# Kernel tuning notes

Hardware: AMD Instinct MI355X
Metric: run time of the kernel (lower is better)

Reference implementation:

```python
import jax, jax.numpy as jnp
import numpy as np

B = 32768    # number of trees (batch)
N = 10       # nodes per tree (forced by Linear(embed_dim*10, ...))
L = 10       # leaf tokens per subtree (also 10, same cat constraint)
E = 16       # embed_dim
H = 8        # hidden_dim
V = 2000     # embed_dict_size
LAT = 128    # latent_vector_dim
EPS = 1e-5   # BatchNorm1d eps


def setup_inputs() -> dict:
    key = jax.random.key(0)
    ks = jax.random.split(key, 17)
    w = lambda k, shape, s=0.05: (jax.random.normal(k, shape, jnp.float32) * s)
    return {
        "tokens": jax.random.randint(ks[0], (B, N, L), 0, V),
        "emb":    w(ks[1], (V, E), 0.1),            # nn.Embedding weight
        "w_ih":   w(ks[2], (4 * E, E)),             # LSTM input weights (i,f,g,o)
        "b_ih":   w(ks[3], (4 * E,)),
        "b_hh":   w(ks[4], (4 * E,)),               # h0=c0=0 so W_hh never contributes
        "ffW1":   w(ks[5], (4 * E, 10 * E)),        # child_sum_ff Linear(160,64)
        "ffb1":   w(ks[6], (4 * E,)),
        "ffW2":   w(ks[7], (E, 4 * E)),             # child_sum_ff Linear(64,16)
        "ffb2":   w(ks[8], (E,)),
        "fmW":    w(ks[9], (H, E)),                 # ff_model Linear(16,8)
        "fmb":    w(ks[10], (H,)),
        "tsW":    w(ks[11], (1, H)),                # tail_score Linear(8,1)
        "tsb":    w(ks[12], (1,)),
        "suW":    w(ks[13], (LAT, H)),              # tail_summary Linear(8,latent)
        "sub_b":  w(ks[14], (LAT,)),
        "gamma":  jnp.ones((LAT,), jnp.float32),    # BatchNorm1d affine
        "beta":   jnp.zeros((LAT,), jnp.float32),
    }


def _child_ff(x, W1, b1, W2, b2):
    # nn.Sequential(Linear(160,64), ReLU, Linear(64,16))
    return jax.nn.relu(x @ W1.T + b1) @ W2.T + b2


def _lstm_single_step(x, w_ih, b_ih, b_hh):
    # One-timestep LSTM with zero initial (h, c); PyTorch gate order i,f,g,o.
    gates = x @ w_ih.T + b_ih + b_hh
    i, f, g, o = jnp.split(gates, 4, axis=-1)
    c = jax.nn.sigmoid(i) * jnp.tanh(g)          # f * c0 = 0
    return jax.nn.sigmoid(o) * jnp.tanh(c)


def reference(tokens, emb, w_ih, b_ih, b_hh, ffW1, ffb1, ffW2, ffb2,
              fmW, fmb, tsW, tsb, suW, sub_b, gamma, beta):
    leaf = emb[tokens]                                        # (B,N,L,E) gather
    subtree = _child_ff(leaf.reshape(B, N, L * E),
                        ffW1, ffb1, ffW2, ffb2)               # (B,N,E)
    h = _lstm_single_step(subtree, w_ih, b_ih, b_hh)          # (B,N,E)
    code = _child_ff(h.reshape(B, N * E), ffW1, ffb1, ffW2, ffb2)  # (B,E)
    ff_out = code @ fmW.T + fmb                               # (B,H)
    score = jnp.tanh(ff_out @ tsW.T + tsb)                    # (B,1)
    s = ff_out @ suW.T + sub_b                                # (B,LAT)
    mu = jnp.mean(s, axis=0)
    var = jnp.var(s, axis=0)                                  # biased, training-mode BN
    summary = gamma * (s - mu) / jnp.sqrt(var + EPS) + beta
    return score, summary
```

## Files before the change

### kernel.cpp

```cpp
#include <hip/hip_runtime.h>
#include <hip/hip_bf16.h>

#define BB 32768
#define NN 10
#define VV 2000
#define EPSBN 1e-5

__global__ __launch_bounds__(256) void k_table(const float* __restrict__ emb,
                                               const float* __restrict__ W1,
                                               float* __restrict__ T1) {
  int idx = blockIdx.x * 256 + threadIdx.x;
  if (idx >= VV * 640) return;
  int v = idx / 640;
  int r = idx - v * 640;
  int l = r >> 6;
  int o = r & 63;
  const float* e = emb + v * 16;
  const float* w = W1 + o * 160 + l * 16;
  float s = 0.f;
#pragma unroll
  for (int k = 0; k < 16; ++k) s = fmaf(e[k], w[k], s);
  T1[idx] = s;
}

__global__ __launch_bounds__(256) void k_fuse(const float* __restrict__ w_ih,
    const float* __restrict__ b_ih, const float* __restrict__ b_hh,
    const float* __restrict__ W2, const float* __restrict__ b2v,
    float* __restrict__ W3, float* __restrict__ bias3) {
  int idx = blockIdx.x * 256 + threadIdx.x;
  if (idx < 4096) {
    int j = idx >> 6, k = idx & 63;
    float s = 0.f;
#pragma unroll
    for (int o = 0; o < 16; ++o) s = fmaf(w_ih[j * 16 + o], W2[o * 64 + k], s);
    W3[idx] = s;
  } else if (idx < 4160) {
    int j = idx - 4096;
    float s = b_ih[j] + b_hh[j];
#pragma unroll
    for (int o = 0; o < 16; ++o) s = fmaf(w_ih[j * 16 + o], b2v[o], s);
    bias3[j] = s;
  }
}

__global__ __launch_bounds__(256) void k_stage1(const int* __restrict__ tokens,
    const float* __restrict__ T1, const float* __restrict__ b1v,
    const float* __restrict__ W3, const float* __restrict__ bias3,
    float* __restrict__ hbuf) {
  __shared__ float lds[4][64];
  const int tid = threadIdx.x;
  const int lane = tid & 63;
  const int wid = tid >> 6;
  float* wl = lds[wid];
  float w3r[64];
#pragma unroll
  for (int k = 0; k < 64; k += 4) {
    float4 v = *(const float4*)&W3[lane * 64 + k];
    w3r[k] = v.x; w3r[k + 1] = v.y; w3r[k + 2] = v.z; w3r[k + 3] = v.w;
  }
  const float b1l = b1v[lane];
  const float b3l = bias3[lane];
  const bool isG = ((lane >> 4) == 2);
  const int gw = blockIdx.x * 4 + wid;

  int item = gw;
  int tokv = (lane < 10) ? tokens[item * 10 + lane] : 0;
  float t[10];
#pragma unroll
  for (int l = 0; l < 10; ++l) {
    int tv = __builtin_amdgcn_readlane(tokv, l);
    t[l] = T1[tv * 640 + l * 64 + lane];
  }
  tokv = (lane < 10) ? tokens[(item + 8192) * 10 + lane] : 0;

  for (int iter = 0; iter < 40; ++iter) {
    float h1 = b1l;
#pragma unroll
    for (int l = 0; l < 10; ++l) h1 += t[l];
    h1 = fmaxf(h1, 0.f);
    wl[lane] = h1;
    __builtin_amdgcn_wave_barrier();

    {
      int tok_n = tokv;
      int nxt2 = item + 16384;
      int src = (nxt2 < BB * NN) ? nxt2 : item;
      tokv = (lane < 10) ? tokens[src * 10 + lane] : 0;
#pragma unroll
      for (int l = 0; l < 10; ++l) {
        int tv = __builtin_amdgcn_readlane(tok_n, l);
        t[l] = T1[tv * 640 + l * 64 + lane];
      }
    }

    float g = b3l;
#pragma unroll
    for (int k = 0; k < 64; k += 4) {
      float4 hv = *(const float4*)&wl[k];
      g = fmaf(w3r[k],     hv.x, g);
      g = fmaf(w3r[k + 1], hv.y, g);
      g = fmaf(w3r[k + 2], hv.z, g);
      g = fmaf(w3r[k + 3], hv.w, g);
    }

    float e = __expf(isG ? -2.f * g : -g);
    float r = 1.f / (1.f + e);
    float act = isG ? fmaf(2.f, r, -1.f) : r;

    int sl = lane & 15;
    float ga = __shfl(act, sl + 32);
    float oa = __shfl(act, sl + 48);
    if (lane < 16) {
      float c = act * ga;
      float e2 = __expf(-2.f * c);
      float th = fmaf(2.f, 1.f / (1.f + e2), -1.f);
      hbuf[item * 16 + lane] = oa * th;
    }
    __builtin_amdgcn_wave_barrier();
    item += 8192;
  }
}

__global__ __launch_bounds__(256) void k_stage2(const float* __restrict__ hbuf,
    const float* __restrict__ W1, const float* __restrict__ b1v,
    const float* __restrict__ W2, const float* __restrict__ b2v,
    const float* __restrict__ fmW, const float* __restrict__ fmb,
    const float* __restrict__ tsW, const float* __restrict__ tsb,
    const float* __restrict__ suW, const float* __restrict__ sub_b,
    float* __restrict__ out, float* __restrict__ partials) {
  __shared__ float h1b_lds[32 * 68];
  __shared__ float code_lds[32 * 20];
  __shared__ float ff_lds[32 * 12];
  int tid = threadIdx.x;
  int lane = tid & 63;
  int wid = __builtin_amdgcn_readfirstlane(tid >> 6);
  int treeBase = blockIdx.x * 32;
  {
    int tw = treeBase + wid * 8;
    float acc[8];
#pragma unroll
    for (int t = 0; t < 8; ++t) acc[t] = b1v[lane];
    const float* wrow = W1 + lane * 160;
    const float* xbase = hbuf + (size_t)tw * 160;
    for (int k = 0; k < 160; k += 4) {
      float4 wv = *(const float4*)(wrow + k);
#pragma unroll
      for (int t = 0; t < 8; ++t) {
        float4 xv = *(const float4*)(xbase + t * 160 + k);
        acc[t] = fmaf(wv.x, xv.x, acc[t]);
        acc[t] = fmaf(wv.y, xv.y, acc[t]);
        acc[t] = fmaf(wv.z, xv.z, acc[t]);
        acc[t] = fmaf(wv.w, xv.w, acc[t]);
      }
    }
#pragma unroll
    for (int t = 0; t < 8; ++t)
      h1b_lds[(wid * 8 + t) * 68 + lane] = fmaxf(acc[t], 0.f);
  }
  __syncthreads();
  {
    int t2 = tid >> 3, jj = tid & 7;
    float c0 = b2v[jj], c1 = b2v[jj + 8];
    const float* w2a = W2 + jj * 64;
    const float* w2b = W2 + (jj + 8) * 64;
    const float* hb = &h1b_lds[t2 * 68];
    for (int o = 0; o < 64; o += 4) {
      float4 hv = *(const float4*)(hb + o);
      float4 a4 = *(const float4*)(w2a + o);
      float4 b4 = *(const float4*)(w2b + o);
      c0 = fmaf(a4.x, hv.x, c0); c0 = fmaf(a4.y, hv.y, c0);
      c0 = fmaf(a4.z, hv.z, c0); c0 = fmaf(a4.w, hv.w, c0);
      c1 = fmaf(b4.x, hv.x, c1); c1 = fmaf(b4.y, hv.y, c1);
      c1 = fmaf(b4.z, hv.z, c1); c1 = fmaf(b4.w, hv.w, c1);
    }
    code_lds[t2 * 20 + jj] = c0;
    code_lds[t2 * 20 + jj + 8] = c1;
  }
  __syncthreads();
  {
    int t = tid >> 3, q = tid & 7;
    float f = fmb[q];
    const float* cw = fmW + q * 16;
    const float* cl = &code_lds[t * 20];
#pragma unroll
    for (int j4 = 0; j4 < 16; j4 += 4) {
      float4 cv = *(const float4*)(cl + j4);
      float4 wv = *(const float4*)(cw + j4);
      f = fmaf(wv.x, cv.x, f); f = fmaf(wv.y, cv.y, f);
      f = fmaf(wv.z, cv.z, f); f = fmaf(wv.w, cv.w, f);
    }
    ff_lds[t * 12 + q] = f;
  }
  __syncthreads();
  {
    int t = tid >> 3, r = tid & 7;
    float4 f0 = *(const float4*)&ff_lds[t * 12];
    float4 f1 = *(const float4*)&ff_lds[t * 12 + 4];
    int tree = treeBase + t;
    float* od = out + (size_t)BB + (size_t)tree * 128 + r * 16;
#pragma unroll
    for (int cc = 0; cc < 16; ++cc) {
      int c = r * 16 + cc;
      const float* u = suW + c * 8;
      float4 u0 = *(const float4*)(u);
      float4 u1 = *(const float4*)(u + 4);
      float sv = sub_b[c];
      sv = fmaf(u0.x, f0.x, sv); sv = fmaf(u0.y, f0.y, sv);
      sv = fmaf(u0.z, f0.z, sv); sv = fmaf(u0.w, f0.w, sv);
      sv = fmaf(u1.x, f1.x, sv); sv = fmaf(u1.y, f1.y, sv);
      sv = fmaf(u1.z, f1.z, sv); sv = fmaf(u1.w, f1.w, sv);
      od[cc] = sv;
    }
    if (tid < 32) {
      int tt = tid;
      float4 g0 = *(const float4*)&ff_lds[tt * 12];
      float4 g1 = *(const float4*)&ff_lds[tt * 12 + 4];
      float sc = tsb[0];
      sc = fmaf(tsW[0], g0.x, sc); sc = fmaf(tsW[1], g0.y, sc);
      sc = fmaf(tsW[2], g0.z, sc); sc = fmaf(tsW[3], g0.w, sc);
      sc = fmaf(tsW[4], g1.x, sc); sc = fmaf(tsW[5], g1.y, sc);
      sc = fmaf(tsW[6], g1.z, sc); sc = fmaf(tsW[7], g1.w, sc);
      out[treeBase + tt] = tanhf(sc);
    }
  }
  {
    int waveId = blockIdx.x * 4 + wid;
    float* pw = partials + (size_t)waveId * 88;
#pragma unroll
    for (int rep = 0; rep < 2; ++rep) {
      int e = lane + rep * 64;
      if (e < 81) {
        int i = e / 9, jx = e - i * 9;
        float m = 0.f;
#pragma unroll
        for (int t = 0; t < 8; ++t) {
          const float* fr = &ff_lds[(wid * 8 + t) * 12];
          float fi = (i  < 8) ? fr[i]  : 1.f;
          float fj = (jx < 8) ? fr[jx] : 1.f;
          m = fmaf(fi, fj, m);
        }
        pw[e] = m;
      }
    }
  }
}

__global__ __launch_bounds__(256) void k_reduce(const float* __restrict__ partials,
                                                double* __restrict__ Msum) {
  __shared__ double red[256];
  int e = blockIdx.x;
  double s = 0.0;
  for (int w = threadIdx.x; w < 4096; w += 256)
    s += (double)partials[(size_t)w * 88 + e];
  red[threadIdx.x] = s;
  __syncthreads();
  for (int off = 128; off > 0; off >>= 1) {
    if (threadIdx.x < off) red[threadIdx.x] += red[threadIdx.x + off];
    __syncthreads();
  }
  if (threadIdx.x == 0) Msum[e] = red[0];
}

__global__ __launch_bounds__(128) void k_stats(const double* __restrict__ Msum,
    const float* __restrict__ suW, const float* __restrict__ sub_b,
    const float* __restrict__ gamma, const float* __restrict__ beta,
    float* __restrict__ statsA, float* __restrict__ statsB) {
  int c = threadIdx.x;
  double u[9];
#pragma unroll
  for (int q = 0; q < 8; ++q) u[q] = (double)suW[c * 8 + q];
  u[8] = (double)sub_b[c];
  double S1 = 0.0;
#pragma unroll
  for (int i = 0; i < 9; ++i) S1 += u[i] * Msum[72 + i];
  double mu = S1 / (double)BB;
  double E2 = 0.0;
#pragma unroll
  for (int i = 0; i < 9; ++i) {
    double acc = 0.0;
#pragma unroll
    for (int jx = 0; jx < 9; ++jx) acc += u[jx] * Msum[i * 9 + jx];
    E2 += u[i] * acc;
  }
  E2 /= (double)BB;
  double var = E2 - mu * mu;
  if (var < 0.0) var = 0.0;
  double rs = 1.0 / sqrt(var + (double)EPSBN);
  double A = (double)gamma[c] * rs;
  statsA[c] = (float)A;
  statsB[c] = (float)((double)beta[c] - mu * A);
}

__global__ __launch_bounds__(256) void k_norm(float* __restrict__ out,
    const float* __restrict__ statsA, const float* __restrict__ statsB) {
  int idx = blockIdx.x * 256 + threadIdx.x;
  float4* p = (float4*)(out + BB);
  float4 v = p[idx];
  int c4 = idx & 31;
  float4 a = ((const float4*)statsA)[c4];
  float4 b = ((const float4*)statsB)[c4];
  v.x = fmaf(v.x, a.x, b.x);
  v.y = fmaf(v.y, a.y, b.y);
  v.z = fmaf(v.z, a.z, b.z);
  v.w = fmaf(v.w, a.w, b.w);
  p[idx] = v;
}

extern "C" void kernel_launch(void* const* d_in, const int* in_sizes, int n_in,
                              void* d_out, int out_size, void* d_ws, size_t ws_size,
                              hipStream_t stream) {
  const int*   tokens = (const int*)d_in[0];
  const float* emb   = (const float*)d_in[1];
  const float* w_ih  = (const float*)d_in[2];
  const float* b_ih  = (const float*)d_in[3];
  const float* b_hh  = (const float*)d_in[4];
  const float* ffW1  = (const float*)d_in[5];
  const float* ffb1  = (const float*)d_in[6];
  const float* ffW2  = (const float*)d_in[7];
  const float* ffb2  = (const float*)d_in[8];
  const float* fmW   = (const float*)d_in[9];
  const float* fmb   = (const float*)d_in[10];
  const float* tsW   = (const float*)d_in[11];
  const float* tsb   = (const float*)d_in[12];
  const float* suW   = (const float*)d_in[13];
  const float* sub_b = (const float*)d_in[14];
  const float* gamma = (const float*)d_in[15];
  const float* beta  = (const float*)d_in[16];
  float* out = (float*)d_out;
  float* ws = (float*)d_ws;

  float*  T1       = ws;
  float*  hbuf     = T1 + 1280000;
  float*  partials = hbuf + 5242880;
  double* Msum     = (double*)(partials + 360448);
  float*  statsA   = (float*)(Msum + 82);
  float*  statsB   = statsA + 128;
  float*  W3       = statsB + 128;
  float*  bias3    = W3 + 4096;

  hipLaunchKernelGGL(k_table,  dim3(5000), dim3(256), 0, stream, emb, ffW1, T1);
  hipLaunchKernelGGL(k_fuse,   dim3(17),   dim3(256), 0, stream,
                     w_ih, b_ih, b_hh, ffW2, ffb2, W3, bias3);
  hipLaunchKernelGGL(k_stage1, dim3(2048), dim3(256), 0, stream,
                     tokens, T1, ffb1, W3, bias3, hbuf);
  hipLaunchKernelGGL(k_stage2, dim3(1024), dim3(256), 0, stream,
                     hbuf, ffW1, ffb1, ffW2, ffb2, fmW, fmb, tsW, tsb, suW, sub_b,
                     out, partials);
  hipLaunchKernelGGL(k_reduce, dim3(81),   dim3(256), 0, stream, partials, Msum);
  hipLaunchKernelGGL(k_stats,  dim3(1),    dim3(128), 0, stream,
                     Msum, suW, sub_b, gamma, beta, statsA, statsB);
  hipLaunchKernelGGL(k_norm,   dim3(4096), dim3(256), 0, stream, out, statsA, statsB);
}
```

Baseline: 195.5 us.

## Double-buffer stage1 gathers with two items in flight and more waves

Restructures the stage-1 node kernel so each wave holds two independent items (tA/tB) and prefetches tokens two items ahead. Token indices are now loaded as uniform scalar loads instead of readlane broadcasts. The grid doubles to 16384 waves with 20 items each, and the launch bounds ask for 4 blocks per CU. Reciprocals switch to the hardware rcp, and an asm barrier pins the W3 weights in registers. The goal is to hide the T1 gather latency; the cost is higher register pressure, which could reduce occupancy or cause spills.

```diff
diff --git a/kernel.cpp b/kernel.cpp
--- a/kernel.cpp
+++ b/kernel.cpp
@@ -43,81 +43,99 @@
   }
 }
 
-__global__ __launch_bounds__(256) void k_stage1(const int* __restrict__ tokens,
+#define K1_WAVES 16384
+#define K1_ITEMS 20
+
+#define K1_STEP(ITEM, T, TOK, NIDX)                                        \
+  {                                                                        \
+    float h1 = b1l;                                                        \
+    _Pragma("unroll") for (int l = 0; l < 10; ++l) h1 += T[l];             \
+    h1 = fmaxf(h1, 0.f);                                                   \
+    wl[lane] = h1;                                                         \
+    __builtin_amdgcn_wave_barrier();                                       \
+    _Pragma("unroll") for (int l = 0; l < 10; ++l) {                       \
+      T[l] = T1[TOK[l] * 640 + l * 64 + lane];                             \
+    }                                                                      \
+    {                                                                      \
+      int ci = (NIDX) < BB * NN ? (NIDX) : 0;                              \
+      const int* tpn = tokens + (size_t)ci * 10;                           \
+      _Pragma("unroll") for (int l = 0; l < 10; ++l) TOK[l] = tpn[l];      \
+    }                                                                      \
+    float g = b3l;                                                         \
+    _Pragma("unroll") for (int k = 0; k < 64; k += 4) {                    \
+      float4 hv = *(const float4*)&wl[k];                                  \
+      g = fmaf(w3r[k],     hv.x, g);                                       \
+      g = fmaf(w3r[k + 1], hv.y, g);                                       \
+      g = fmaf(w3r[k + 2], hv.z, g);                                       \
+      g = fmaf(w3r[k + 3], hv.w, g);                                       \
+    }                                                                      \
+    float e = __expf(isG ? -2.f * g : -g);                                 \
+    float r = __builtin_amdgcn_rcpf(1.f + e);                              \
+    float act = isG ? fmaf(2.f, r, -1.f) : r;                              \
+    int sl = lane & 15;                                                    \
+    float ga = __shfl(act, sl + 32);                                       \
+    float oa = __shfl(act, sl + 48);                                       \
+    if (lane < 16) {                                                       \
+      float c = act * ga;                                                  \
+      float e2 = __expf(-2.f * c);                                         \
+      float th = fmaf(2.f, __builtin_amdgcn_rcpf(1.f + e2), -1.f);         \
+      hbuf[(size_t)(ITEM) * 16 + lane] = oa * th;                          \
+    }                                                                      \
+    __builtin_amdgcn_wave_barrier();                                       \
+  }
+
+__global__ __launch_bounds__(256, 4) void k_stage1(const int* __restrict__ tokens,
     const float* __restrict__ T1, const float* __restrict__ b1v,
     const float* __restrict__ W3, const float* __restrict__ bias3,
     float* __restrict__ hbuf) {
   __shared__ float lds[4][64];
   const int tid = threadIdx.x;
   const int lane = tid & 63;
-  const int wid = tid >> 6;
+  const int wid = __builtin_amdgcn_readfirstlane(tid >> 6);
   float* wl = lds[wid];
+
   float w3r[64];
 #pragma unroll
   for (int k = 0; k < 64; k += 4) {
     float4 v = *(const float4*)&W3[lane * 64 + k];
     w3r[k] = v.x; w3r[k + 1] = v.y; w3r[k + 2] = v.z; w3r[k + 3] = v.w;
   }
+#pragma unroll
+  for (int k = 0; k < 64; ++k) asm volatile("" : "+v"(w3r[k]));
+
   const float b1l = b1v[lane];
   const float b3l = bias3[lane];
   const bool isG = ((lane >> 4) == 2);
-  const int gw = blockIdx.x * 4 + wid;
-
-  int item = gw;
-  int tokv = (lane < 10) ? tokens[item * 10 + lane] : 0;
-  float t[10];
-#pragma unroll
-  for (int l = 0; l < 10; ++l) {
-    int tv = __builtin_amdgcn_readlane(tokv, l);
-    t[l] = T1[tv * 640 + l * 64 + lane];
-  }
-  tokv = (lane < 10) ? tokens[(item + 8192) * 10 + lane] : 0;
-
-  for (int iter = 0; iter < 40; ++iter) {
-    float h1 = b1l;
-#pragma unroll
-    for (int l = 0; l < 10; ++l) h1 += t[l];
-    h1 = fmaxf(h1, 0.f);
-    wl[lane] = h1;
-    __builtin_amdgcn_wave_barrier();
-
-    {
-      int tok_n = tokv;
-      int nxt2 = item + 16384;
-      int src = (nxt2 < BB * NN) ? nxt2 : item;
-      tokv = (lane < 10) ? tokens[src * 10 + lane] : 0;
-#pragma unroll
-      for (int l = 0; l < 10; ++l) {
-        int tv = __builtin_amdgcn_readlane(tok_n, l);
-        t[l] = T1[tv * 640 + l * 64 + lane];
-      }
-    }
-
-    float g = b3l;
-#pragma unroll
-    for (int k = 0; k < 64; k += 4) {
-      float4 hv = *(const float4*)&wl[k];
-      g = fmaf(w3r[k],     hv.x, g);
-      g = fmaf(w3r[k + 1], hv.y, g);
-      g = fmaf(w3r[k + 2], hv.z, g);
-      g = fmaf(w3r[k + 3], hv.w, g);
-    }
-
-    float e = __expf(isG ? -2.f * g : -g);
-    float r = 1.f / (1.f + e);
-    float act = isG ? fmaf(2.f, r, -1.f) : r;
-
-    int sl = lane & 15;
-    float ga = __shfl(act, sl + 32);
-    float oa = __shfl(act, sl + 48);
-    if (lane < 16) {
-      float c = act * ga;
-      float e2 = __expf(-2.f * c);
-      float th = fmaf(2.f, 1.f / (1.f + e2), -1.f);
-      hbuf[item * 16 + lane] = oa * th;
-    }
-    __builtin_amdgcn_wave_barrier();
-    item += 8192;
+  const int gw = __builtin_amdgcn_readfirstlane(blockIdx.x * 4 + wid);
+
+  int tokA[10], tokB[10];
+  float tA[10], tB[10];
+  {
+    const int* t0 = tokens + (size_t)gw * 10;
+    const int* t1 = tokens + (size_t)(gw + K1_WAVES) * 10;
+#pragma unroll
+    for (int l = 0; l < 10; ++l) tokA[l] = t0[l];
+#pragma unroll
+    for (int l = 0; l < 10; ++l) tokB[l] = t1[l];
+  }
+#pragma unroll
+  for (int l = 0; l < 10; ++l) tA[l] = T1[tokA[l] * 640 + l * 64 + lane];
+#pragma unroll
+  for (int l = 0; l < 10; ++l) tB[l] = T1[tokB[l] * 640 + l * 64 + lane];
+  {
+    const int* t2 = tokens + (size_t)(gw + 2 * K1_WAVES) * 10;
+    const int* t3 = tokens + (size_t)(gw + 3 * K1_WAVES) * 10;
+#pragma unroll
+    for (int l = 0; l < 10; ++l) tokA[l] = t2[l];
+#pragma unroll
+    for (int l = 0; l < 10; ++l) tokB[l] = t3[l];
+  }
+
+#pragma unroll 1
+  for (int it = 0; it < K1_ITEMS; it += 2) {
+    int item = gw + it * K1_WAVES;
+    K1_STEP(item, tA, tokA, gw + (it + 4) * K1_WAVES);
+    K1_STEP(item + K1_WAVES, tB, tokB, gw + (it + 5) * K1_WAVES);
   }
 }
 
@@ -341,7 +359,7 @@
   hipLaunchKernelGGL(k_table,  dim3(5000), dim3(256), 0, stream, emb, ffW1, T1);
   hipLaunchKernelGGL(k_fuse,   dim3(17),   dim3(256), 0, stream,
                      w_ih, b_ih, b_hh, ffW2, ffb2, W3, bias3);
-  hipLaunchKernelGGL(k_stage1, dim3(2048), dim3(256), 0, stream,
+  hipLaunchKernelGGL(k_stage1, dim3(4096), dim3(256), 0, stream,
                      tokens, T1, ffb1, W3, bias3, hbuf);
   hipLaunchKernelGGL(k_stage2, dim3(1024), dim3(256), 0, stream,
                      hbuf, ffW1, ffb1, ffW2, ffb2, fmW, fmb, tsW, tsb, suW, sub_b,
```

New measurement: 186.5 us. 1.05x faster.

## Map one subtree item per thread in stage1 and drop the unused forget gate

Applied to the files above, without the earlier changes.

Stage1 moves from one wave per item, where lanes hold hidden units and share activations through LDS and shuffles, to one thread per item. Each thread gathers full 64-wide T1 rows with float4 loads, computes the 48 needed gate outputs (the forget gate is dropped from the fused weights) and writes 16 outputs with vector stores. This removes LDS traffic, wave barriers and cross-lane shuffles and cuts gate work by a quarter. In exchange each lane reads 640-float scattered rows, so gather coalescing gets worse. Register pressure is also high (64 h1 plus accumulators), and the W3T reads are uniform broadcast loads.

```diff
diff --git a/kernel.cpp b/kernel.cpp
--- a/kernel.cpp
+++ b/kernel.cpp
@@ -26,98 +26,106 @@
 __global__ __launch_bounds__(256) void k_fuse(const float* __restrict__ w_ih,
     const float* __restrict__ b_ih, const float* __restrict__ b_hh,
     const float* __restrict__ W2, const float* __restrict__ b2v,
-    float* __restrict__ W3, float* __restrict__ bias3) {
+    float* __restrict__ W3T, float* __restrict__ bias3T) {
   int idx = blockIdx.x * 256 + threadIdx.x;
-  if (idx < 4096) {
-    int j = idx >> 6, k = idx & 63;
+  if (idx < 3072) {
+    int k = idx / 48, jj = idx - k * 48;
+    int gr = (jj < 16) ? jj : jj + 16;
     float s = 0.f;
 #pragma unroll
-    for (int o = 0; o < 16; ++o) s = fmaf(w_ih[j * 16 + o], W2[o * 64 + k], s);
-    W3[idx] = s;
-  } else if (idx < 4160) {
-    int j = idx - 4096;
-    float s = b_ih[j] + b_hh[j];
-#pragma unroll
-    for (int o = 0; o < 16; ++o) s = fmaf(w_ih[j * 16 + o], b2v[o], s);
-    bias3[j] = s;
-  }
-}
-
-__global__ __launch_bounds__(256) void k_stage1(const int* __restrict__ tokens,
+    for (int o = 0; o < 16; ++o) s = fmaf(w_ih[gr * 16 + o], W2[o * 64 + k], s);
+    W3T[idx] = s;
+  } else if (idx < 3120) {
+    int jj = idx - 3072;
+    int gr = (jj < 16) ? jj : jj + 16;
+    float s = b_ih[gr] + b_hh[gr];
+#pragma unroll
+    for (int o = 0; o < 16; ++o) s = fmaf(w_ih[gr * 16 + o], b2v[o], s);
+    bias3T[jj] = s;
+  }
+}
+
+__global__ __launch_bounds__(64, 2) void k_stage1(const int* __restrict__ tokens,
     const float* __restrict__ T1, const float* __restrict__ b1v,
-    const float* __restrict__ W3, const float* __restrict__ bias3,
+    const float* __restrict__ W3T, const float* __restrict__ bias3T,
     float* __restrict__ hbuf) {
-  __shared__ float lds[4][64];
-  const int tid = threadIdx.x;
-  const int lane = tid & 63;
-  const int wid = tid >> 6;
-  float* wl = lds[wid];
-  float w3r[64];
-#pragma unroll
-  for (int k = 0; k < 64; k += 4) {
-    float4 v = *(const float4*)&W3[lane * 64 + k];
-    w3r[k] = v.x; w3r[k + 1] = v.y; w3r[k + 2] = v.z; w3r[k + 3] = v.w;
-  }
-  const float b1l = b1v[lane];
-  const float b3l = bias3[lane];
-  const bool isG = ((lane >> 4) == 2);
-  const int gw = blockIdx.x * 4 + wid;
-
-  int item = gw;
-  int tokv = (lane < 10) ? tokens[item * 10 + lane] : 0;
-  float t[10];
-#pragma unroll
-  for (int l = 0; l < 10; ++l) {
-    int tv = __builtin_amdgcn_readlane(tokv, l);
-    t[l] = T1[tv * 640 + l * 64 + lane];
-  }
-  tokv = (lane < 10) ? tokens[(item + 8192) * 10 + lane] : 0;
-
-  for (int iter = 0; iter < 40; ++iter) {
-    float h1 = b1l;
-#pragma unroll
-    for (int l = 0; l < 10; ++l) h1 += t[l];
-    h1 = fmaxf(h1, 0.f);
-    wl[lane] = h1;
-    __builtin_amdgcn_wave_barrier();
-
+  const int lane = threadIdx.x;
+#pragma unroll 1
+  for (int b = 0; b < 2; ++b) {
+    const int item = (blockIdx.x * 2 + b) * 64 + lane;
+    const int* tp = tokens + (size_t)item * 10;
+    int tok[10];
+#pragma unroll
+    for (int l = 0; l < 10; ++l) tok[l] = tp[l];
+
+    float4 h[16];
     {
-      int tok_n = tokv;
-      int nxt2 = item + 16384;
-      int src = (nxt2 < BB * NN) ? nxt2 : item;
-      tokv = (lane < 10) ? tokens[src * 10 + lane] : 0;
-#pragma unroll
-      for (int l = 0; l < 10; ++l) {
-        int tv = __builtin_amdgcn_readlane(tok_n, l);
-        t[l] = T1[tv * 640 + l * 64 + lane];
-      }
-    }
-
-    float g = b3l;
-#pragma unroll
-    for (int k = 0; k < 64; k += 4) {
-      float4 hv = *(const float4*)&wl[k];
-      g = fmaf(w3r[k],     hv.x, g);
-      g = fmaf(w3r[k + 1], hv.y, g);
-      g = fmaf(w3r[k + 2], hv.z, g);
-      g = fmaf(w3r[k + 3], hv.w, g);
-    }
-
-    float e = __expf(isG ? -2.f * g : -g);
-    float r = 1.f / (1.f + e);
-    float act = isG ? fmaf(2.f, r, -1.f) : r;
-
-    int sl = lane & 15;
-    float ga = __shfl(act, sl + 32);
-    float oa = __shfl(act, sl + 48);
-    if (lane < 16) {
-      float c = act * ga;
+      const float4* r = (const float4*)(T1 + (size_t)tok[0] * 640);
+#pragma unroll
+      for (int c = 0; c < 16; ++c) h[c] = r[c];
+    }
+#pragma unroll
+    for (int l = 1; l < 10; ++l) {
+      const float4* r = (const float4*)(T1 + (size_t)tok[l] * 640 + l * 64);
+#pragma unroll
+      for (int c = 0; c < 16; ++c) {
+        float4 v = r[c];
+        h[c].x += v.x; h[c].y += v.y; h[c].z += v.z; h[c].w += v.w;
+      }
+    }
+    float h1[64];
+    const float4* b1q = (const float4*)b1v;
+#pragma unroll
+    for (int c = 0; c < 16; ++c) {
+      float4 bq = b1q[c];
+      h1[4 * c]     = fmaxf(h[c].x + bq.x, 0.f);
+      h1[4 * c + 1] = fmaxf(h[c].y + bq.y, 0.f);
+      h1[4 * c + 2] = fmaxf(h[c].z + bq.z, 0.f);
+      h1[4 * c + 3] = fmaxf(h[c].w + bq.w, 0.f);
+    }
+
+    float acti[16], actg[16], acto[16];
+#pragma unroll
+    for (int ch = 0; ch < 3; ++ch) {
+      float acc[16];
+#pragma unroll
+      for (int j = 0; j < 16; ++j) acc[j] = bias3T[ch * 16 + j];
+#pragma unroll
+      for (int k = 0; k < 64; ++k) {
+        const float hk = h1[k];
+#pragma unroll
+        for (int j = 0; j < 16; ++j)
+          acc[j] = fmaf(W3T[k * 48 + ch * 16 + j], hk, acc[j]);
+      }
+#pragma unroll
+      for (int j = 0; j < 16; ++j) {
+        float x = acc[j];
+        float a;
+        if (ch == 1) {
+          float e = __expf(-2.f * x);
+          a = fmaf(2.f, __builtin_amdgcn_rcpf(1.f + e), -1.f);
+        } else {
+          float e = __expf(-x);
+          a = __builtin_amdgcn_rcpf(1.f + e);
+        }
+        if (ch == 0) acti[j] = a;
+        else if (ch == 1) actg[j] = a;
+        else acto[j] = a;
+      }
+    }
+
+    float res[16];
+#pragma unroll
+    for (int j = 0; j < 16; ++j) {
+      float c = acti[j] * actg[j];
       float e2 = __expf(-2.f * c);
-      float th = fmaf(2.f, 1.f / (1.f + e2), -1.f);
-      hbuf[item * 16 + lane] = oa * th;
-    }
-    __builtin_amdgcn_wave_barrier();
-    item += 8192;
+      float th = fmaf(2.f, __builtin_amdgcn_rcpf(1.f + e2), -1.f);
+      res[j] = acto[j] * th;
+    }
+    float4* op = (float4*)(hbuf + (size_t)item * 16);
+#pragma unroll
+    for (int q = 0; q < 4; ++q)
+      op[q] = make_float4(res[4 * q], res[4 * q + 1], res[4 * q + 2], res[4 * q + 3]);
   }
 }
 
@@ -335,14 +343,14 @@
   double* Msum     = (double*)(partials + 360448);
   float*  statsA   = (float*)(Msum + 82);
   float*  statsB   = statsA + 128;
-  float*  W3       = statsB + 128;
-  float*  bias3    = W3 + 4096;
+  float*  W3T      = statsB + 128;
+  float*  bias3T   = W3T + 3072;
 
   hipLaunchKernelGGL(k_table,  dim3(5000), dim3(256), 0, stream, emb, ffW1, T1);
-  hipLaunchKernelGGL(k_fuse,   dim3(17),   dim3(256), 0, stream,
-                     w_ih, b_ih, b_hh, ffW2, ffb2, W3, bias3);
-  hipLaunchKernelGGL(k_stage1, dim3(2048), dim3(256), 0, stream,
-                     tokens, T1, ffb1, W3, bias3, hbuf);
+  hipLaunchKernelGGL(k_fuse,   dim3(13),   dim3(256), 0, stream,
+                     w_ih, b_ih, b_hh, ffW2, ffb2, W3T, bias3T);
+  hipLaunchKernelGGL(k_stage1, dim3(2560), dim3(64), 0, stream,
+                     tokens, T1, ffb1, W3T, bias3T, hbuf);
   hipLaunchKernelGGL(k_stage2, dim3(1024), dim3(256), 0, stream,
                      hbuf, ffW1, ffb1, ffW2, ffb2, fmW, fmb, tsW, tsb, suW, sub_b,
                      out, partials);
```

Result: slower. 384.1 us (+96.4%).

## Split stage1 into gather kernel and batched gate kernel, merge prep kernels

Applied to the files above, without the earlier changes.

Replaces the persistent stage-1 kernel with two kernels: one gathers and sums table rows with float4 loads into an h1 buffer (folding the b1 bias into the table), and one computes the LSTM gates for 8 items per wave, reusing each weight load across them. The two small precompute kernels are merged into one launch, and division is replaced with hardware reciprocal. This trades the fused register pipeline for an extra intermediate buffer (about 84 MB written and read back) in exchange for more parallelism and better weight reuse.

```diff
diff --git a/kernel.cpp b/kernel.cpp
--- a/kernel.cpp
+++ b/kernel.cpp
@@ -6,118 +6,109 @@
 #define VV 2000
 #define EPSBN 1e-5
 
-__global__ __launch_bounds__(256) void k_table(const float* __restrict__ emb,
-                                               const float* __restrict__ W1,
-                                               float* __restrict__ T1) {
+__global__ __launch_bounds__(256) void k_prep(const float* __restrict__ emb,
+    const float* __restrict__ W1, const float* __restrict__ b1v,
+    const float* __restrict__ w_ih, const float* __restrict__ b_ih,
+    const float* __restrict__ b_hh, const float* __restrict__ W2,
+    const float* __restrict__ b2v,
+    float* __restrict__ T1, float* __restrict__ W3R, float* __restrict__ bias3) {
+  if (blockIdx.x < 5000) {
+    int idx = blockIdx.x * 256 + threadIdx.x;
+    int v = idx / 640;
+    int r = idx - v * 640;
+    int l = r >> 6;
+    int o = r & 63;
+    const float* e = emb + v * 16;
+    const float* w = W1 + o * 160 + l * 16;
+    float s = (l == 0) ? b1v[o] : 0.f;
+#pragma unroll
+    for (int k = 0; k < 16; ++k) s = fmaf(e[k], w[k], s);
+    T1[idx] = s;
+  } else {
+    int idx = (blockIdx.x - 5000) * 256 + threadIdx.x;
+    if (idx < 4096) {
+      int j = idx >> 6, k = idx & 63;
+      float s = 0.f;
+#pragma unroll
+      for (int o = 0; o < 16; ++o) s = fmaf(w_ih[j * 16 + o], W2[o * 64 + k], s);
+      W3R[idx] = s;
+    } else if (idx < 4160) {
+      int j = idx - 4096;
+      float s = b_ih[j] + b_hh[j];
+#pragma unroll
+      for (int o = 0; o < 16; ++o) s = fmaf(w_ih[j * 16 + o], b2v[o], s);
+      bias3[j] = s;
+    }
+  }
+}
+
+__global__ __launch_bounds__(256) void k_h1(const int* __restrict__ tokens,
+    const float* __restrict__ T1, float* __restrict__ h1buf) {
   int idx = blockIdx.x * 256 + threadIdx.x;
-  if (idx >= VV * 640) return;
-  int v = idx / 640;
-  int r = idx - v * 640;
-  int l = r >> 6;
-  int o = r & 63;
-  const float* e = emb + v * 16;
-  const float* w = W1 + o * 160 + l * 16;
-  float s = 0.f;
-#pragma unroll
-  for (int k = 0; k < 16; ++k) s = fmaf(e[k], w[k], s);
-  T1[idx] = s;
-}
-
-__global__ __launch_bounds__(256) void k_fuse(const float* __restrict__ w_ih,
-    const float* __restrict__ b_ih, const float* __restrict__ b_hh,
-    const float* __restrict__ W2, const float* __restrict__ b2v,
-    float* __restrict__ W3, float* __restrict__ bias3) {
-  int idx = blockIdx.x * 256 + threadIdx.x;
-  if (idx < 4096) {
-    int j = idx >> 6, k = idx & 63;
-    float s = 0.f;
-#pragma unroll
-    for (int o = 0; o < 16; ++o) s = fmaf(w_ih[j * 16 + o], W2[o * 64 + k], s);
-    W3[idx] = s;
-  } else if (idx < 4160) {
-    int j = idx - 4096;
-    float s = b_ih[j] + b_hh[j];
-#pragma unroll
-    for (int o = 0; o < 16; ++o) s = fmaf(w_ih[j * 16 + o], b2v[o], s);
-    bias3[j] = s;
-  }
-}
-
-__global__ __launch_bounds__(256) void k_stage1(const int* __restrict__ tokens,
-    const float* __restrict__ T1, const float* __restrict__ b1v,
-    const float* __restrict__ W3, const float* __restrict__ bias3,
+  int item = idx >> 4, c4 = (idx & 15) * 4;
+  const int* tp = tokens + (size_t)item * 10;
+  float4 a;
+  {
+    const float4* r = (const float4*)(T1 + (size_t)tp[0] * 640 + c4);
+    a = *r;
+  }
+#pragma unroll
+  for (int l = 1; l < 10; ++l) {
+    const float4* r = (const float4*)(T1 + (size_t)tp[l] * 640 + l * 64 + c4);
+    float4 v = *r;
+    a.x += v.x; a.y += v.y; a.z += v.z; a.w += v.w;
+  }
+  a.x = fmaxf(a.x, 0.f); a.y = fmaxf(a.y, 0.f);
+  a.z = fmaxf(a.z, 0.f); a.w = fmaxf(a.w, 0.f);
+  ((float4*)h1buf)[idx] = a;
+}
+
+__global__ __launch_bounds__(256) void k_gates(const float* __restrict__ h1buf,
+    const float* __restrict__ W3R, const float* __restrict__ bias3,
     float* __restrict__ hbuf) {
-  __shared__ float lds[4][64];
   const int tid = threadIdx.x;
   const int lane = tid & 63;
-  const int wid = tid >> 6;
-  float* wl = lds[wid];
-  float w3r[64];
-#pragma unroll
+  const int wid = __builtin_amdgcn_readfirstlane(tid >> 6);
+  const int itemBase = blockIdx.x * 32 + wid * 8;
+  const float* wrow = W3R + lane * 64;
+  const float* xb = h1buf + (size_t)itemBase * 64;
+
+  float acc[8];
+  {
+    float b = bias3[lane];
+#pragma unroll
+    for (int t = 0; t < 8; ++t) acc[t] = b;
+  }
   for (int k = 0; k < 64; k += 4) {
-    float4 v = *(const float4*)&W3[lane * 64 + k];
-    w3r[k] = v.x; w3r[k + 1] = v.y; w3r[k + 2] = v.z; w3r[k + 3] = v.w;
-  }
-  const float b1l = b1v[lane];
-  const float b3l = bias3[lane];
+    float4 wv = *(const float4*)(wrow + k);
+#pragma unroll
+    for (int t = 0; t < 8; ++t) {
+      float4 xv = *(const float4*)(xb + t * 64 + k);
+      acc[t] = fmaf(wv.x, xv.x, acc[t]);
+      acc[t] = fmaf(wv.y, xv.y, acc[t]);
+      acc[t] = fmaf(wv.z, xv.z, acc[t]);
+      acc[t] = fmaf(wv.w, xv.w, acc[t]);
+    }
+  }
   const bool isG = ((lane >> 4) == 2);
-  const int gw = blockIdx.x * 4 + wid;
-
-  int item = gw;
-  int tokv = (lane < 10) ? tokens[item * 10 + lane] : 0;
-  float t[10];
-#pragma unroll
-  for (int l = 0; l < 10; ++l) {
-    int tv = __builtin_amdgcn_readlane(tokv, l);
-    t[l] = T1[tv * 640 + l * 64 + lane];
-  }
-  tokv = (lane < 10) ? tokens[(item + 8192) * 10 + lane] : 0;
-
-  for (int iter = 0; iter < 40; ++iter) {
-    float h1 = b1l;
-#pragma unroll
-    for (int l = 0; l < 10; ++l) h1 += t[l];
-    h1 = fmaxf(h1, 0.f);
-    wl[lane] = h1;
-    __builtin_amdgcn_wave_barrier();
-
-    {
-      int tok_n = tokv;
-      int nxt2 = item + 16384;
-      int src = (nxt2 < BB * NN) ? nxt2 : item;
-      tokv = (lane < 10) ? tokens[src * 10 + lane] : 0;
-#pragma unroll
-      for (int l = 0; l < 10; ++l) {
-        int tv = __builtin_amdgcn_readlane(tok_n, l);
-        t[l] = T1[tv * 640 + l * 64 + lane];
-      }
-    }
-
-    float g = b3l;
-#pragma unroll
-    for (int k = 0; k < 64; k += 4) {
-      float4 hv = *(const float4*)&wl[k];
-      g = fmaf(w3r[k],     hv.x, g);
-      g = fmaf(w3r[k + 1], hv.y, g);
-      g = fmaf(w3r[k + 2], hv.z, g);
-      g = fmaf(w3r[k + 3], hv.w, g);
-    }
-
-    float e = __expf(isG ? -2.f * g : -g);
-    float r = 1.f / (1.f + e);
-    float act = isG ? fmaf(2.f, r, -1.f) : r;
-
-    int sl = lane & 15;
-    float ga = __shfl(act, sl + 32);
-    float oa = __shfl(act, sl + 48);
+#pragma unroll
+  for (int t = 0; t < 8; ++t) {
+    float x = acc[t];
+    float e = __expf(isG ? -2.f * x : -x);
+    float r = __builtin_amdgcn_rcpf(1.f + e);
+    acc[t] = isG ? fmaf(2.f, r, -1.f) : r;
+  }
+  const int sl = lane & 15;
+#pragma unroll
+  for (int t = 0; t < 8; ++t) {
+    float ga = __shfl(acc[t], sl + 32);
+    float oa = __shfl(acc[t], sl + 48);
     if (lane < 16) {
-      float c = act * ga;
+      float c = acc[t] * ga;
       float e2 = __expf(-2.f * c);
-      float th = fmaf(2.f, 1.f / (1.f + e2), -1.f);
-      hbuf[item * 16 + lane] = oa * th;
-    }
-    __builtin_amdgcn_wave_barrier();
-    item += 8192;
+      float th = fmaf(2.f, __builtin_amdgcn_rcpf(1.f + e2), -1.f);
+      hbuf[(size_t)(itemBase + t) * 16 + lane] = oa * th;
+    }
   }
 }
 
@@ -335,19 +326,20 @@
   double* Msum     = (double*)(partials + 360448);
   float*  statsA   = (float*)(Msum + 82);
   float*  statsB   = statsA + 128;
-  float*  W3       = statsB + 128;
-  float*  bias3    = W3 + 4096;
-
-  hipLaunchKernelGGL(k_table,  dim3(5000), dim3(256), 0, stream, emb, ffW1, T1);
-  hipLaunchKernelGGL(k_fuse,   dim3(17),   dim3(256), 0, stream,
-                     w_ih, b_ih, b_hh, ffW2, ffb2, W3, bias3);
-  hipLaunchKernelGGL(k_stage1, dim3(2048), dim3(256), 0, stream,
-                     tokens, T1, ffb1, W3, bias3, hbuf);
-  hipLaunchKernelGGL(k_stage2, dim3(1024), dim3(256), 0, stream,
+  float*  W3R      = statsB + 128;
+  float*  bias3    = W3R + 4096;
+  float*  h1buf    = bias3 + 60 + 4;
+
+  hipLaunchKernelGGL(k_prep,   dim3(5017),  dim3(256), 0, stream,
+                     emb, ffW1, ffb1, w_ih, b_ih, b_hh, ffW2, ffb2, T1, W3R, bias3);
+  hipLaunchKernelGGL(k_h1,     dim3(20480), dim3(256), 0, stream, tokens, T1, h1buf);
+  hipLaunchKernelGGL(k_gates,  dim3(10240), dim3(256), 0, stream,
+                     h1buf, W3R, bias3, hbuf);
+  hipLaunchKernelGGL(k_stage2, dim3(1024),  dim3(256), 0, stream,
                      hbuf, ffW1, ffb1, ffW2, ffb2, fmW, fmb, tsW, tsb, suW, sub_b,
                      out, partials);
-  hipLaunchKernelGGL(k_reduce, dim3(81),   dim3(256), 0, stream, partials, Msum);
-  hipLaunchKernelGGL(k_stats,  dim3(1),    dim3(128), 0, stream,
+  hipLaunchKernelGGL(k_reduce, dim3(81),    dim3(256), 0, stream, partials, Msum);
+  hipLaunchKernelGGL(k_stats,  dim3(1),     dim3(128), 0, stream,
                      Msum, suW, sub_b, gamma, beta, statsA, statsB);
-  hipLaunchKernelGGL(k_norm,   dim3(4096), dim3(256), 0, stream, out, statsA, statsB);
-}
+  hipLaunchKernelGGL(k_norm,   dim3(4096),  dim3(256), 0, stream, out, statsA, statsB);
+}
```

Result: slower. 235.1 us (+20.2%).
